# Optimization experiments

Hardware: AMD Instinct MI355X
Metric: run time of the kernel (lower is better)

## Reference

```python
import jax, jax.numpy as jnp
import numpy as np

E4M3_MAX = 448.0
M, K, N = 131072, 512, 512


def _round_to_fp8_e4m3(x):
    # Emulated round-to-nearest E4M3: 3 mantissa bits, exponent in [-7, 8]
    abs_x = jnp.abs(x)
    sign = jnp.sign(x)
    exponent = jnp.clip(jnp.floor(jnp.log2(jnp.maximum(abs_x, 2.0 ** -9))), -7.0, 8.0)
    pow2e = jnp.exp2(exponent)
    mantissa = jnp.round(abs_x / pow2e * 8.0) / 8.0  # jnp.round is half-to-even, matching torch.round
    return sign * mantissa * pow2e


def _quantize_e4m3(x, scale):
    scaled = jnp.clip(x * scale, -E4M3_MAX, E4M3_MAX)
    return _round_to_fp8_e4m3(scaled)


def _dynamic_scale(x):
    # FP8TensorMeta.compute_scale with a single amax in history: max_value / amax * 0.9
    amax = jnp.max(jnp.abs(x))
    return jnp.where(amax > 0, E4M3_MAX / amax * 0.9, 1.0)


def setup_inputs() -> dict:
    key = jax.random.key(0)
    k1, k2, k3 = jax.random.split(key, 3)
    bound = 1.0 / np.sqrt(K)  # kaiming_uniform(a=sqrt(5)) on [N,K] -> U(-1/sqrt(K), 1/sqrt(K))
    x = jax.random.normal(k1, (M, K), dtype=jnp.float32)
    weight = jax.random.uniform(k2, (N, K), dtype=jnp.float32, minval=-bound, maxval=bound)
    bias = jax.random.uniform(k3, (N,), dtype=jnp.float32, minval=-bound, maxval=bound)
    return {"x": x, "weight": weight, "bias": bias}


def reference(x, weight, bias):
    input_scale = _dynamic_scale(x)
    weight_scale = _dynamic_scale(weight)
    x_fp8 = _quantize_e4m3(x, input_scale)          # [M, K]
    w_fp8 = _quantize_e4m3(weight, weight_scale)    # [N, K]
    out = jnp.einsum("mk,nk->mn", x_fp8, w_fp8) + bias  # F.linear
    return out / (input_scale * weight_scale)
```

## Files before the change

kernel.cpp:

```cpp
#include <hip/hip_runtime.h>

typedef unsigned short u16;
typedef unsigned int u32;
typedef unsigned char u8;
typedef __attribute__((ext_vector_type(4))) float f32x4;

template <bool HI>
__device__ __forceinline__ u32 q2fp8(float a, float b, u32 old, float s) {
  a = fminf(448.0f, fmaxf(-448.0f, a * s));
  b = fminf(448.0f, fmaxf(-448.0f, b * s));
  return (u32)__builtin_amdgcn_cvt_pk_fp8_f32(a, b, (int)old, HI);
}

__device__ __forceinline__ float block_max(float m) {
#pragma unroll
  for (int off = 32; off > 0; off >>= 1)
    m = fmaxf(m, __shfl_down(m, off, 64));
  __shared__ float sm[4];
  int wv = threadIdx.x >> 6;
  if ((threadIdx.x & 63) == 0) sm[wv] = m;
  __syncthreads();
  float r = fmaxf(fmaxf(sm[0], sm[1]), fmaxf(sm[2], sm[3]));
  __syncthreads();
  return r;
}

#define XBLOCKS 2048
#define WBLOCKS 64

__global__ void amax2_kernel(const float4* __restrict__ x, int nx4,
                             const float4* __restrict__ w, int nw4,
                             float* __restrict__ px, float* __restrict__ pw) {
  int bid = blockIdx.x;
  const float4* p;
  int n4, b, nb;
  float* dst;
  if (bid < XBLOCKS) { p = x; n4 = nx4; dst = px; b = bid; nb = XBLOCKS; }
  else { p = w; n4 = nw4; dst = pw; b = bid - XBLOCKS; nb = WBLOCKS; }
  float m = 0.0f;
  int stride = nb * 256;
  for (int i = b * 256 + threadIdx.x; i < n4; i += stride) {
    float4 v = p[i];
    m = fmaxf(m, fmaxf(fmaxf(fabsf(v.x), fabsf(v.y)), fmaxf(fabsf(v.z), fabsf(v.w))));
  }
  m = block_max(m);
  if (threadIdx.x == 0) dst[b] = m;
}

__device__ __forceinline__ float wave_max64(float m) {
#pragma unroll
  for (int off = 32; off > 0; off >>= 1) m = fmaxf(m, __shfl_xor(m, off, 64));
  return m;
}

__global__ void quant_w_kernel(const float* __restrict__ w, u8* __restrict__ wq,
                               const float* __restrict__ pw) {
  float mw = wave_max64(pw[threadIdx.x & 63]);
  const float sw = mw > 0.0f ? 448.0f / mw * 0.9f : 1.0f;
  const int id = blockIdx.x * blockDim.x + threadIdx.x;
  const int kc = id >> 9;
  const int n = id & 511;
  const float4* src = (const float4*)(w + (size_t)n * 512 + kc * 8);
  const float4 a = src[0];
  const float4 b = src[1];
  uint2 r;
  r.x = q2fp8<false>(a.x, a.y, 0u, sw);
  r.x = q2fp8<true>(a.z, a.w, r.x, sw);
  r.y = q2fp8<false>(b.x, b.y, 0u, sw);
  r.y = q2fp8<true>(b.z, b.w, r.y, sw);
  *(uint2*)&wq[(size_t)kc * 4096 + n * 8] = r;
}

__global__ void __launch_bounds__(512, 4) gemm_kernel(const float* __restrict__ x,
                                                      const u8* __restrict__ wq,
                                                      const float* __restrict__ bias,
                                                      float* __restrict__ out,
                                                      const float* __restrict__ px,
                                                      const float* __restrict__ pw) {
  __shared__ __align__(16) u8 As[2 * 8192];
  __shared__ __align__(16) u8 Bs[3 * 16384];
  __shared__ float sm8[8];
  const int tid = threadIdx.x;
  const int lane = tid & 63;
  const int wv = tid >> 6;
  const int quad = lane >> 4;
  const int lr = lane & 15;

  const int lin = blockIdx.x;
  const int xcd = lin & 7;
  const int jn = (lin >> 3) & 1;
  const int grp = lin >> 4;
  const int m0 = (grp * 8 + xcd) * 128;
  const int n0 = jn * 256;

  const int wm = (wv >> 2) * 64;
  const int wn = (wv & 3) * 64;
  const int xrow = tid >> 2;
  const int xc = tid & 3;

  f32x4 acc[4][4] = {};
  float4 xr[2][4];

  float pxv[4];
#pragma unroll
  for (int i = 0; i < 4; ++i) pxv[i] = px[tid + i * 512];
  float pwv = pw[lane];

  auto stageB = [&](int bu, int kt) {
#pragma unroll
    for (int i = 0; i < 2; ++i) {
      const u8* gp = wq + (size_t)(kt * 8 + wv) * 4096 + (size_t)n0 * 8 + i * 1024 + lane * 16;
      u8* lp = &Bs[bu * 16384 + wv * 2048 + i * 1024 + lane * 16];
      __builtin_amdgcn_global_load_lds((const __attribute__((address_space(1))) u32*)gp,
                                       (__attribute__((address_space(3))) u32*)lp, 16, 0, 0);
    }
  };
  auto loadX = [&](int slot, int kt) {
    const float* p = x + (size_t)(m0 + xrow) * 512 + kt * 64 + xc * 16;
#pragma unroll
    for (int s = 0; s < 4; ++s) xr[slot][s] = *(const float4*)(p + s * 4);
  };

  loadX(0, 0);
  loadX(1, 1);
  stageB(0, 0);
  stageB(1, 1);

  float m = fmaxf(fmaxf(pxv[0], pxv[1]), fmaxf(pxv[2], pxv[3]));
  m = wave_max64(m);
  if (lane == 0) sm8[wv] = m;
  __syncthreads();
  float mx = sm8[0];
#pragma unroll
  for (int i = 1; i < 8; ++i) mx = fmaxf(mx, sm8[i]);
  float mw = wave_max64(pwv);
  const float sx = mx > 0.0f ? 448.0f / mx * 0.9f : 1.0f;
  const float sw = mw > 0.0f ? 448.0f / mw * 0.9f : 1.0f;
  const float inv = 1.0f / (sx * sw);

  auto writeA = [&](int bu, int slot) {
    uint4 pk;
    pk.x = q2fp8<false>(xr[slot][0].x, xr[slot][0].y, 0u, sx);
    pk.x = q2fp8<true>(xr[slot][0].z, xr[slot][0].w, pk.x, sx);
    pk.y = q2fp8<false>(xr[slot][1].x, xr[slot][1].y, 0u, sx);
    pk.y = q2fp8<true>(xr[slot][1].z, xr[slot][1].w, pk.y, sx);
    pk.z = q2fp8<false>(xr[slot][2].x, xr[slot][2].y, 0u, sx);
    pk.z = q2fp8<true>(xr[slot][2].z, xr[slot][2].w, pk.z, sx);
    pk.w = q2fp8<false>(xr[slot][3].x, xr[slot][3].y, 0u, sx);
    pk.w = q2fp8<true>(xr[slot][3].z, xr[slot][3].w, pk.w, sx);
    *(uint4*)&As[bu * 8192 + xc * 2048 + xrow * 16] = pk;
  };

  writeA(0, 0);
  asm volatile("s_waitcnt vmcnt(2) lgkmcnt(0)" ::: "memory");
  __builtin_amdgcn_s_barrier();
  asm volatile("" ::: "memory");

#pragma unroll
  for (int kt = 0; kt < 8; ++kt) {
    const int cur3 = kt % 3;
    const int curA = kt & 1;
    if (kt < 6) {
      loadX(kt & 1, kt + 2);
      stageB((kt + 2) % 3, kt + 2);
    }
#pragma unroll
    for (int kk = 0; kk < 2; ++kk) {
      long af[4], bf[4];
#pragma unroll
      for (int mi = 0; mi < 4; ++mi)
        af[mi] = *(const long*)&As[curA * 8192 + (kk * 2 + (quad >> 1)) * 2048 +
                                   (wm + mi * 16 + lr) * 16 + (quad & 1) * 8];
#pragma unroll
      for (int ni = 0; ni < 4; ++ni)
        bf[ni] = *(const long*)&Bs[cur3 * 16384 + (kk * 4 + quad) * 2048 + (wn + ni * 16 + lr) * 8];
      __builtin_amdgcn_s_setprio(1);
#pragma unroll
      for (int mi = 0; mi < 4; ++mi)
#pragma unroll
        for (int ni = 0; ni < 4; ++ni)
          acc[mi][ni] = __builtin_amdgcn_mfma_f32_16x16x32_fp8_fp8(af[mi], bf[ni], acc[mi][ni], 0, 0, 0);
      __builtin_amdgcn_s_setprio(0);
    }
    if (kt < 7) {
      writeA(curA ^ 1, (kt + 1) & 1);
      if (kt < 6) {
        asm volatile("s_waitcnt vmcnt(6) lgkmcnt(0)" ::: "memory");
      } else {
        asm volatile("s_waitcnt vmcnt(0) lgkmcnt(0)" ::: "memory");
      }
      __builtin_amdgcn_s_barrier();
      asm volatile("" ::: "memory");
    }
  }

  float bn[4];
#pragma unroll
  for (int ni = 0; ni < 4; ++ni) bn[ni] = bias[n0 + wn + ni * 16 + lr];
#pragma unroll
  for (int mi = 0; mi < 4; ++mi) {
    const int gr = m0 + wm + mi * 16 + quad * 4;
#pragma unroll
    for (int ni = 0; ni < 4; ++ni) {
      const int gc = n0 + wn + ni * 16 + lr;
#pragma unroll
      for (int j = 0; j < 4; ++j)
        out[(size_t)(gr + j) * 512 + gc] = (acc[mi][ni][j] + bn[ni]) * inv;
    }
  }
}

extern "C" void kernel_launch(void* const* d_in, const int* in_sizes, int n_in,
                              void* d_out, int out_size, void* d_ws, size_t ws_size,
                              hipStream_t stream) {
  const float* x = (const float*)d_in[0];
  const float* w = (const float*)d_in[1];
  const float* bias = (const float*)d_in[2];
  float* out = (float*)d_out;

  const int K = 512, N = 512;
  const int M = in_sizes[0] / K;

  float* ws_f = (float*)d_ws;
  float* px = ws_f + 16;
  float* pw = ws_f + 16 + XBLOCKS;
  u8* wq = (u8*)((char*)d_ws + 16384);

  hipLaunchKernelGGL(amax2_kernel, dim3(XBLOCKS + WBLOCKS), dim3(256), 0, stream,
                     (const float4*)x, (M * K) / 4, (const float4*)w, (N * K) / 4, px, pw);
  hipLaunchKernelGGL(quant_w_kernel, dim3((N * K / 8) / 256), dim3(256), 0, stream,
                     w, wq, pw);
  hipLaunchKernelGGL(gemm_kernel, dim3((M / 128) * 2), dim3(512), 0, stream,
                     x, wq, bias, out, px, pw);
}
```

Before: 561.6 us.

## Shrink GEMM tile to 64x128 with 256 threads and pre-quantized X registers

Shrinks the GEMM block tile from 128x256 (512 threads) to 64x128 (256 threads), giving four N-tiles per M-strip and raising target occupancy. The X prefetch changes from two raw float4 register slots to one raw slot plus two quantized uint4 slots, so quantization is done early and the LDS write only stores packed bytes. Smaller tiles mean x is re-read from global memory four times instead of twice, and there is less data reuse per MFMA.

```diff
diff --git a/kernel.cpp b/kernel.cpp
--- a/kernel.cpp
+++ b/kernel.cpp
@@ -71,15 +71,15 @@
   *(uint2*)&wq[(size_t)kc * 4096 + n * 8] = r;
 }
 
-__global__ void __launch_bounds__(512, 4) gemm_kernel(const float* __restrict__ x,
+__global__ void __launch_bounds__(256, 5) gemm_kernel(const float* __restrict__ x,
                                                       const u8* __restrict__ wq,
                                                       const float* __restrict__ bias,
                                                       float* __restrict__ out,
                                                       const float* __restrict__ px,
                                                       const float* __restrict__ pw) {
-  __shared__ __align__(16) u8 As[2 * 8192];
-  __shared__ __align__(16) u8 Bs[3 * 16384];
-  __shared__ float sm8[8];
+  __shared__ __align__(16) u8 As[2 * 4096];
+  __shared__ __align__(16) u8 Bs[3 * 8192];
+  float* smf = (float*)&Bs[2 * 8192];
   const int tid = threadIdx.x;
   const int lane = tid & 63;
   const int wv = tid >> 6;
@@ -88,71 +88,81 @@
 
   const int lin = blockIdx.x;
   const int xcd = lin & 7;
-  const int jn = (lin >> 3) & 1;
-  const int grp = lin >> 4;
-  const int m0 = (grp * 8 + xcd) * 128;
-  const int n0 = jn * 256;
-
-  const int wm = (wv >> 2) * 64;
-  const int wn = (wv & 3) * 64;
+  const int rest = lin >> 3;
+  const int jn = rest & 3;
+  const int grp = rest >> 2;
+  const int m0 = (grp * 8 + xcd) * 64;
+  const int n0 = jn * 128;
+
+  const int wm = (wv >> 1) * 32;
+  const int wn = (wv & 1) * 64;
   const int xrow = tid >> 2;
   const int xc = tid & 3;
 
-  f32x4 acc[4][4] = {};
-  float4 xr[2][4];
-
-  float pxv[4];
-#pragma unroll
-  for (int i = 0; i < 4; ++i) pxv[i] = px[tid + i * 512];
+  f32x4 acc[2][4] = {};
+  float4 xr[4];
+  uint4 xq[2];
+
+  float pxv[8];
+#pragma unroll
+  for (int i = 0; i < 8; ++i) pxv[i] = px[tid + i * 256];
   float pwv = pw[lane];
 
   auto stageB = [&](int bu, int kt) {
 #pragma unroll
     for (int i = 0; i < 2; ++i) {
-      const u8* gp = wq + (size_t)(kt * 8 + wv) * 4096 + (size_t)n0 * 8 + i * 1024 + lane * 16;
-      u8* lp = &Bs[bu * 16384 + wv * 2048 + i * 1024 + lane * 16];
+      const int c = wv * 2 + i;
+      const u8* gp = wq + (size_t)(kt * 8 + c) * 4096 + (size_t)n0 * 8 + lane * 16;
+      u8* lp = &Bs[bu * 8192 + c * 1024 + lane * 16];
       __builtin_amdgcn_global_load_lds((const __attribute__((address_space(1))) u32*)gp,
                                        (__attribute__((address_space(3))) u32*)lp, 16, 0, 0);
     }
   };
-  auto loadX = [&](int slot, int kt) {
+  auto loadX = [&](int kt) {
     const float* p = x + (size_t)(m0 + xrow) * 512 + kt * 64 + xc * 16;
 #pragma unroll
-    for (int s = 0; s < 4; ++s) xr[slot][s] = *(const float4*)(p + s * 4);
-  };
-
-  loadX(0, 0);
-  loadX(1, 1);
+    for (int s = 0; s < 4; ++s) xr[s] = *(const float4*)(p + s * 4);
+  };
+
+  loadX(0);
   stageB(0, 0);
   stageB(1, 1);
 
-  float m = fmaxf(fmaxf(pxv[0], pxv[1]), fmaxf(pxv[2], pxv[3]));
+  float m = pxv[0];
+#pragma unroll
+  for (int i = 1; i < 8; ++i) m = fmaxf(m, pxv[i]);
   m = wave_max64(m);
-  if (lane == 0) sm8[wv] = m;
-  __syncthreads();
-  float mx = sm8[0];
-#pragma unroll
-  for (int i = 1; i < 8; ++i) mx = fmaxf(mx, sm8[i]);
+  if (lane == 0) smf[wv] = m;
+  asm volatile("s_waitcnt lgkmcnt(0)" ::: "memory");
+  __builtin_amdgcn_s_barrier();
+  float mx = fmaxf(fmaxf(smf[0], smf[1]), fmaxf(smf[2], smf[3]));
   float mw = wave_max64(pwv);
   const float sx = mx > 0.0f ? 448.0f / mx * 0.9f : 1.0f;
   const float sw = mw > 0.0f ? 448.0f / mw * 0.9f : 1.0f;
   const float inv = 1.0f / (sx * sw);
-
+  __builtin_amdgcn_s_barrier();
+
+  auto quantX = [&](int slot) {
+    uint4 pk;
+    pk.x = q2fp8<false>(xr[0].x, xr[0].y, 0u, sx);
+    pk.x = q2fp8<true>(xr[0].z, xr[0].w, pk.x, sx);
+    pk.y = q2fp8<false>(xr[1].x, xr[1].y, 0u, sx);
+    pk.y = q2fp8<true>(xr[1].z, xr[1].w, pk.y, sx);
+    pk.z = q2fp8<false>(xr[2].x, xr[2].y, 0u, sx);
+    pk.z = q2fp8<true>(xr[2].z, xr[2].w, pk.z, sx);
+    pk.w = q2fp8<false>(xr[3].x, xr[3].y, 0u, sx);
+    pk.w = q2fp8<true>(xr[3].z, xr[3].w, pk.w, sx);
+    xq[slot] = pk;
+  };
   auto writeA = [&](int bu, int slot) {
-    uint4 pk;
-    pk.x = q2fp8<false>(xr[slot][0].x, xr[slot][0].y, 0u, sx);
-    pk.x = q2fp8<true>(xr[slot][0].z, xr[slot][0].w, pk.x, sx);
-    pk.y = q2fp8<false>(xr[slot][1].x, xr[slot][1].y, 0u, sx);
-    pk.y = q2fp8<true>(xr[slot][1].z, xr[slot][1].w, pk.y, sx);
-    pk.z = q2fp8<false>(xr[slot][2].x, xr[slot][2].y, 0u, sx);
-    pk.z = q2fp8<true>(xr[slot][2].z, xr[slot][2].w, pk.z, sx);
-    pk.w = q2fp8<false>(xr[slot][3].x, xr[slot][3].y, 0u, sx);
-    pk.w = q2fp8<true>(xr[slot][3].z, xr[slot][3].w, pk.w, sx);
-    *(uint4*)&As[bu * 8192 + xc * 2048 + xrow * 16] = pk;
-  };
-
+    *(uint4*)&As[bu * 4096 + xc * 1024 + xrow * 16] = xq[slot];
+  };
+
+  quantX(0);
   writeA(0, 0);
-  asm volatile("s_waitcnt vmcnt(2) lgkmcnt(0)" ::: "memory");
+  loadX(1);
+  quantX(1);
+  asm volatile("s_waitcnt lgkmcnt(0)" ::: "memory");
   __builtin_amdgcn_s_barrier();
   asm volatile("" ::: "memory");
 
@@ -161,31 +171,32 @@
     const int cur3 = kt % 3;
     const int curA = kt & 1;
     if (kt < 6) {
-      loadX(kt & 1, kt + 2);
+      loadX(kt + 2);
       stageB((kt + 2) % 3, kt + 2);
     }
 #pragma unroll
     for (int kk = 0; kk < 2; ++kk) {
-      long af[4], bf[4];
-#pragma unroll
-      for (int mi = 0; mi < 4; ++mi)
-        af[mi] = *(const long*)&As[curA * 8192 + (kk * 2 + (quad >> 1)) * 2048 +
+      long af[2], bf[4];
+#pragma unroll
+      for (int mi = 0; mi < 2; ++mi)
+        af[mi] = *(const long*)&As[curA * 4096 + (kk * 2 + (quad >> 1)) * 1024 +
                                    (wm + mi * 16 + lr) * 16 + (quad & 1) * 8];
 #pragma unroll
       for (int ni = 0; ni < 4; ++ni)
-        bf[ni] = *(const long*)&Bs[cur3 * 16384 + (kk * 4 + quad) * 2048 + (wn + ni * 16 + lr) * 8];
+        bf[ni] = *(const long*)&Bs[cur3 * 8192 + (kk * 4 + quad) * 1024 + (wn + ni * 16 + lr) * 8];
       __builtin_amdgcn_s_setprio(1);
 #pragma unroll
-      for (int mi = 0; mi < 4; ++mi)
+      for (int mi = 0; mi < 2; ++mi)
 #pragma unroll
         for (int ni = 0; ni < 4; ++ni)
           acc[mi][ni] = __builtin_amdgcn_mfma_f32_16x16x32_fp8_fp8(af[mi], bf[ni], acc[mi][ni], 0, 0, 0);
       __builtin_amdgcn_s_setprio(0);
     }
+    if (kt < 6) quantX(kt & 1);
     if (kt < 7) {
       writeA(curA ^ 1, (kt + 1) & 1);
       if (kt < 6) {
-        asm volatile("s_waitcnt vmcnt(6) lgkmcnt(0)" ::: "memory");
+        asm volatile("s_waitcnt vmcnt(2) lgkmcnt(0)" ::: "memory");
       } else {
         asm volatile("s_waitcnt vmcnt(0) lgkmcnt(0)" ::: "memory");
       }
@@ -198,7 +209,7 @@
 #pragma unroll
   for (int ni = 0; ni < 4; ++ni) bn[ni] = bias[n0 + wn + ni * 16 + lr];
 #pragma unroll
-  for (int mi = 0; mi < 4; ++mi) {
+  for (int mi = 0; mi < 2; ++mi) {
     const int gr = m0 + wm + mi * 16 + quad * 4;
 #pragma unroll
     for (int ni = 0; ni < 4; ++ni) {
@@ -230,6 +241,6 @@
                      (const float4*)x, (M * K) / 4, (const float4*)w, (N * K) / 4, px, pw);
   hipLaunchKernelGGL(quant_w_kernel, dim3((N * K / 8) / 256), dim3(256), 0, stream,
                      w, wq, pw);
-  hipLaunchKernelGGL(gemm_kernel, dim3((M / 128) * 2), dim3(512), 0, stream,
+  hipLaunchKernelGGL(gemm_kernel, dim3((M / 64) * (N / 128)), dim3(256), 0, stream,
                      x, wq, bias, out, px, pw);
 }
```

Result: faster. 542.4 us (-3.4%).
